# Kernel optimization log

Hardware: AMD Instinct MI355X
Metric: run time of the kernel (lower is better)

The kernel has to match this reference:

```python
import jax, jax.numpy as jnp
import numpy as np

T, B, I, H = 512, 256, 256, 256


def setup_inputs() -> dict:
    key = jax.random.key(0)
    ks = jax.random.split(key, 4)
    s = 1.0 / np.sqrt(I + H)  # fan-in scaling like nn.Linear default
    return {
        "x": jax.random.normal(ks[0], (T, B, I), dtype=jnp.float32),
        "h": jnp.zeros((B, H), dtype=jnp.float32),
        "Wz_w": jax.random.normal(ks[1], (H, I + H), dtype=jnp.float32) * s,
        "Wz_b": jnp.zeros((H,), dtype=jnp.float32),
        "Wr_w": jax.random.normal(ks[2], (H, I + H), dtype=jnp.float32) * s,
        "Wr_b": jnp.zeros((H,), dtype=jnp.float32),
        "W_w": jax.random.normal(ks[3], (H, I + H), dtype=jnp.float32) * s,
        "W_b": jnp.zeros((H,), dtype=jnp.float32),
    }


def reference(x, h, Wz_w, Wz_b, Wr_w, Wr_b, W_w, W_b):
    # x: [T, B, I], h: [B, H]. Gate input order is cat(h, x) as in the torch code.
    def step(h, xt):
        gate = jnp.concatenate([h, xt], axis=1)              # [B, H+I]
        zt = jax.nn.sigmoid(gate @ Wz_w.T + Wz_b)            # [B, H]
        rt = jax.nn.sigmoid(gate @ Wr_w.T + Wr_b)            # [B, H]
        cand_in = jnp.concatenate([rt * h, xt], axis=1)      # [B, H+I]
        ht = (1.0 - zt) * h + zt * jnp.tanh(cand_in @ W_w.T + W_b)
        return ht, ht

    h_final, hAll = jax.lax.scan(step, h, x)                 # hAll: [T, B, H]
    return hAll, h_final
```

## Files before the change

### kernel.cpp

```cpp
#include <hip/hip_runtime.h>


typedef float f32x4 __attribute__((ext_vector_type(4)));
typedef short bf16x8 __attribute__((ext_vector_type(8)));

__device__ __forceinline__ unsigned short f2bf(float f) {
  union { float f; unsigned int u; } v; v.f = f;
  unsigned int u = v.u + 0x7fffu + ((v.u >> 16) & 1u);
  return (unsigned short)(u >> 16);
}
__device__ __forceinline__ float u2f(unsigned int u) {
  union { unsigned int u; float f; } v; v.u = u; return v.f;
}
__device__ __forceinline__ unsigned int cvt_pk_bf16(float lo, float hi) {
  unsigned int r;
  asm("v_cvt_pk_bf16_f32 %0, %1, %2" : "=v"(r) : "v"(lo), "v"(hi));
  return r;
}
__device__ __forceinline__ float sigmoid_f(float x) {
  return __builtin_amdgcn_rcpf(1.f + __expf(-x));
}
__device__ __forceinline__ float tanh_f(float x) {
  float e = __expf(2.f * x);
  return 1.f - 2.f * __builtin_amdgcn_rcpf(e + 1.f);
}
__device__ __forceinline__ f32x4 unpk(uint2 gv) {
  f32x4 a;
  a[0] = u2f(gv.x << 16); a[1] = u2f(gv.x & 0xffff0000u);
  a[2] = u2f(gv.y << 16); a[3] = u2f(gv.y & 0xffff0000u);
  return a;
}

__global__ __launch_bounds__(256) void gru_gx_kernel(
    const float* __restrict__ x,
    const float* __restrict__ Wz, const float* __restrict__ Wr, const float* __restrict__ Wc,
    const float* __restrict__ bz, const float* __restrict__ br, const float* __restrict__ bc,
    unsigned short* __restrict__ gx)
{
  __shared__ __align__(16) unsigned short As[64][72];
  __shared__ __align__(16) unsigned short Bs[64][72];

  const int tid  = threadIdx.x;
  const int lane = tid & 63;
  const int wid  = tid >> 6;
  const int l15  = lane & 15;
  const int lg   = lane >> 4;
  const int m0   = blockIdx.x * 64;
  const int by   = blockIdx.y;
  const int gate = by >> 2;
  const int jb   = (by & 3) * 64;
  const float* W    = (gate == 0) ? Wz : ((gate == 1) ? Wr : Wc);
  const float* bias = (gate == 0) ? bz : ((gate == 1) ? br : bc);

  f32x4 acc[4];
  #pragma unroll
  for (int n = 0; n < 4; ++n) acc[n] = (f32x4){0.f, 0.f, 0.f, 0.f};

  for (int k0 = 0; k0 < 256; k0 += 64) {
    #pragma unroll
    for (int i = 0; i < 4; ++i) {
      int idx = tid + i * 256;
      int row = idx >> 4;
      int kq  = (idx & 15) << 2;
      float4 va = *(const float4*)(x + (size_t)(m0 + row) * 256 + k0 + kq);
      ushort4 ua; ua.x = f2bf(va.x); ua.y = f2bf(va.y); ua.z = f2bf(va.z); ua.w = f2bf(va.w);
      *(ushort4*)&As[row][kq] = ua;
      float4 vb = *(const float4*)(W + (size_t)(jb + row) * 512 + 256 + k0 + kq);
      ushort4 ub; ub.x = f2bf(vb.x); ub.y = f2bf(vb.y); ub.z = f2bf(vb.z); ub.w = f2bf(vb.w);
      *(ushort4*)&Bs[row][kq] = ub;
    }
    __syncthreads();
    #pragma unroll
    for (int ks = 0; ks < 64; ks += 32) {
      bf16x8 af = *(const bf16x8*)&As[wid * 16 + l15][ks + lg * 8];
      #pragma unroll
      for (int n = 0; n < 4; ++n) {
        bf16x8 bf = *(const bf16x8*)&Bs[n * 16 + l15][ks + lg * 8];
        acc[n] = __builtin_amdgcn_mfma_f32_16x16x32_bf16(af, bf, acc[n], 0, 0, 0);
      }
    }
    __syncthreads();
  }

  #pragma unroll
  for (int n = 0; n < 4; ++n) {
    float bv = bias[jb + n * 16 + l15];
    #pragma unroll
    for (int r = 0; r < 4; ++r) {
      As[wid * 16 + lg * 4 + r][n * 16 + l15] = f2bf(acc[n][r] + bv);
    }
  }
  __syncthreads();

  const int tt    = m0 >> 8;
  const int b0    = m0 & 255;
  const int jbase = by * 64;
  #pragma unroll
  for (int i = 0; i < 2; ++i) {
    int u    = tid + i * 256;
    int bg_l = u >> 7;
    int rem  = u & 127;
    int cb_l = rem >> 3;
    int bp   = rem & 7;
    int row0 = bg_l * 16 + bp * 2;
    uint2 lo = *(const uint2*)&As[row0][cb_l * 4];
    uint2 hi = *(const uint2*)&As[row0 + 1][cb_l * 4];
    uint4 val; val.x = lo.x; val.y = lo.y; val.z = hi.x; val.w = hi.y;
    size_t off = (((size_t)tt * 16 + (b0 >> 4) + bg_l) * 192 + (jbase >> 2) + cb_l) * 64
                 + (size_t)bp * 8;
    *(uint4*)(gx + off) = val;
  }
}

__global__ __launch_bounds__(512, 1) void gru_rec_kernel(
    const unsigned short* __restrict__ gx,
    const float* __restrict__ h0,
    const float* __restrict__ Wz, const float* __restrict__ Wr, const float* __restrict__ Wc,
    float* __restrict__ out)
{
  __shared__ __align__(16) float h_s[16][260];
  __shared__ __align__(16) float zt_s[16][260];
  __shared__ __align__(16) unsigned short hA[16][264];
  __shared__ __align__(16) unsigned short rhA[16][264];

  const int tid   = threadIdx.x;
  const int lane  = tid & 63;
  const int wid   = tid >> 6;
  const int l15   = lane & 15;
  const int lg    = lane >> 4;
  const int wg    = blockIdx.x;
  const int brow0 = wg * 16;

  bf16x8 w1[4][8];
  {
    const float* W  = (wid < 4) ? Wz : Wr;
    const int    cb = (wid & 3) * 64;
    #pragma unroll
    for (int n = 0; n < 4; ++n) {
      const int j = cb + n * 16 + l15;
      #pragma unroll
      for (int kk = 0; kk < 8; ++kk) {
        const int k = kk * 32 + lg * 8;
        const float* p = W + (size_t)j * 512 + k;
        float4 a = *(const float4*)p;
        float4 b = *(const float4*)(p + 4);
        bf16x8 f;
        f[0] = (short)f2bf(a.x); f[1] = (short)f2bf(a.y);
        f[2] = (short)f2bf(a.z); f[3] = (short)f2bf(a.w);
        f[4] = (short)f2bf(b.x); f[5] = (short)f2bf(b.y);
        f[6] = (short)f2bf(b.z); f[7] = (short)f2bf(b.w);
        w1[n][kk] = f;
      }
    }
  }
  bf16x8 w2[2][8];
  {
    const int cb = wid * 32;
    #pragma unroll
    for (int n = 0; n < 2; ++n) {
      const int j = cb + n * 16 + l15;
      #pragma unroll
      for (int kk = 0; kk < 8; ++kk) {
        const int k = kk * 32 + lg * 8;
        const float* p = Wc + (size_t)j * 512 + k;
        float4 a = *(const float4*)p;
        float4 b = *(const float4*)(p + 4);
        bf16x8 f;
        f[0] = (short)f2bf(a.x); f[1] = (short)f2bf(a.y);
        f[2] = (short)f2bf(a.z); f[3] = (short)f2bf(a.w);
        f[4] = (short)f2bf(b.x); f[5] = (short)f2bf(b.y);
        f[6] = (short)f2bf(b.z); f[7] = (short)f2bf(b.w);
        w2[n][kk] = f;
      }
    }
  }

  for (int idx = tid; idx < 16 * 256; idx += 512) {
    int r = idx >> 8, c = idx & 255;
    float v = h0[(size_t)(brow0 + r) * 256 + c];
    h_s[r][c] = v;
    hA[r][c]  = f2bf(v);
  }

  uint2 g1[4], g2[2];
  {
    const size_t tb = (size_t)wg * 12288;
    #pragma unroll
    for (int n = 0; n < 4; ++n)
      g1[n] = *(const uint2*)(gx + tb + (size_t)(wid * 16 + n * 4 + lg) * 64 + l15 * 4);
    #pragma unroll
    for (int n = 0; n < 2; ++n)
      g2[n] = *(const uint2*)(gx + tb + (size_t)(128 + wid * 8 + n * 4 + lg) * 64 + l15 * 4);
  }
  __syncthreads();

  for (int t = 0; t < 512; ++t) {
    const int tn = (t < 511) ? (t + 1) : 511;
    const size_t tbn = ((size_t)tn * 16 + wg) * 12288;

    const int cb1 = wid * 64;
    f32x4 acc[4];
    #pragma unroll
    for (int n = 0; n < 4; ++n) acc[n] = unpk(g1[n]);
    #pragma unroll
    for (int n = 0; n < 4; ++n)
      g1[n] = *(const uint2*)(gx + tbn + (size_t)(wid * 16 + n * 4 + lg) * 64 + l15 * 4);

    #pragma unroll
    for (int kk = 0; kk < 8; ++kk) {
      bf16x8 hf = *(const bf16x8*)&hA[l15][kk * 32 + lg * 8];
      #pragma unroll
      for (int n = 0; n < 4; ++n)
        acc[n] = __builtin_amdgcn_mfma_f32_16x16x32_bf16(w1[n][kk], hf, acc[n], 0, 0, 0);
    }
    if (wid < 4) {
      #pragma unroll
      for (int n = 0; n < 4; ++n) {
        const int c0 = cb1 + n * 16 + lg * 4;
        f32x4 zv;
        #pragma unroll
        for (int r = 0; r < 4; ++r) zv[r] = sigmoid_f(acc[n][r]);
        *(f32x4*)&zt_s[l15][c0] = zv;
      }
    } else {
      #pragma unroll
      for (int n = 0; n < 4; ++n) {
        const int c0h = (cb1 - 256) + n * 16 + lg * 4;
        f32x4 hv = *(const f32x4*)&h_s[l15][c0h];
        float rh0 = sigmoid_f(acc[n][0]) * hv[0];
        float rh1 = sigmoid_f(acc[n][1]) * hv[1];
        float rh2 = sigmoid_f(acc[n][2]) * hv[2];
        float rh3 = sigmoid_f(acc[n][3]) * hv[3];
        uint2 pk; pk.x = cvt_pk_bf16(rh0, rh1); pk.y = cvt_pk_bf16(rh2, rh3);
        *(uint2*)&rhA[l15][c0h] = pk;
      }
    }
    asm volatile("s_waitcnt lgkmcnt(0)" ::: "memory");
    __builtin_amdgcn_s_barrier();
    __builtin_amdgcn_sched_barrier(0);

    f32x4 acc2[2];
    #pragma unroll
    for (int n = 0; n < 2; ++n) acc2[n] = unpk(g2[n]);
    #pragma unroll
    for (int n = 0; n < 2; ++n)
      g2[n] = *(const uint2*)(gx + tbn + (size_t)(128 + wid * 8 + n * 4 + lg) * 64 + l15 * 4);

    #pragma unroll
    for (int kk = 0; kk < 8; ++kk) {
      bf16x8 rf = *(const bf16x8*)&rhA[l15][kk * 32 + lg * 8];
      #pragma unroll
      for (int n = 0; n < 2; ++n)
        acc2[n] = __builtin_amdgcn_mfma_f32_16x16x32_bf16(w2[n][kk], rf, acc2[n], 0, 0, 0);
    }
    #pragma unroll
    for (int n = 0; n < 2; ++n) {
      const int j0 = wid * 32 + n * 16 + lg * 4;
      f32x4 zv = *(const f32x4*)&zt_s[l15][j0];
      f32x4 hp = *(const f32x4*)&h_s[l15][j0];
      f32x4 ht;
      #pragma unroll
      for (int r = 0; r < 4; ++r) {
        float th = tanh_f(acc2[n][r]);
        ht[r] = hp[r] + zv[r] * (th - hp[r]);
      }
      *(f32x4*)(out + (size_t)t * 65536 + (size_t)(brow0 + l15) * 256 + j0) = ht;
      if (t == 511)
        *(f32x4*)(out + (size_t)33554432 + (size_t)(brow0 + l15) * 256 + j0) = ht;
      *(f32x4*)&h_s[l15][j0] = ht;
      uint2 pk; pk.x = cvt_pk_bf16(ht[0], ht[1]); pk.y = cvt_pk_bf16(ht[2], ht[3]);
      *(uint2*)&hA[l15][j0] = pk;
    }
    asm volatile("s_waitcnt lgkmcnt(0)" ::: "memory");
    __builtin_amdgcn_s_barrier();
    __builtin_amdgcn_sched_barrier(0);
  }
}

extern "C" void kernel_launch(void* const* d_in, const int* in_sizes, int n_in,
                              void* d_out, int out_size, void* d_ws, size_t ws_size,
                              hipStream_t stream) {
  const float* x  = (const float*)d_in[0];
  const float* h0 = (const float*)d_in[1];
  const float* Wz = (const float*)d_in[2];
  const float* bz = (const float*)d_in[3];
  const float* Wr = (const float*)d_in[4];
  const float* br = (const float*)d_in[5];
  const float* Wc = (const float*)d_in[6];
  const float* bc = (const float*)d_in[7];
  float* out = (float*)d_out;
  unsigned short* gxbuf = (unsigned short*)d_ws;

  dim3 gridA(2048, 12);
  gru_gx_kernel<<<gridA, 256, 0, stream>>>(x, Wz, Wr, Wc, bz, br, bc, gxbuf);
  gru_rec_kernel<<<16, 512, 0, stream>>>(gxbuf, h0, Wz, Wr, Wc, out);
}
```

Measured before the change: 1.272 ms.

## Store h in MFMA fragment order, split accumulator chains, raise MFMA priority

The bf16 hidden-state buffers hA and rhA now use an MFMA-fragment-ordered layout, so each lane reads its 8-element B operand as a contiguous 16-byte chunk at lane*8 instead of a strided row access. The K loop of both recurrent GEMMs is split into two independent accumulator chains that are summed before the activation, which shortens the dependent MFMA chain on the serial critical path. s_setprio raises wave priority around the MFMA blocks. The writes become scattered 8-byte stores through frag_off, and the extra accumulators raise register pressure.

```diff
diff --git a/kernel.cpp b/kernel.cpp
--- a/kernel.cpp
+++ b/kernel.cpp
@@ -29,6 +29,9 @@
   a[0] = u2f(gv.x << 16); a[1] = u2f(gv.x & 0xffff0000u);
   a[2] = u2f(gv.y << 16); a[3] = u2f(gv.y & 0xffff0000u);
   return a;
+}
+__device__ __forceinline__ int frag_off(int j, int b) {
+  return ((j >> 5) * 64 + ((j >> 3) & 3) * 16 + b) * 8 + (j & 7);
 }
 
 __global__ __launch_bounds__(256) void gru_gx_kernel(
@@ -120,8 +123,8 @@
 {
   __shared__ __align__(16) float h_s[16][260];
   __shared__ __align__(16) float zt_s[16][260];
-  __shared__ __align__(16) unsigned short hA[16][264];
-  __shared__ __align__(16) unsigned short rhA[16][264];
+  __shared__ __align__(16) unsigned short hA[4096];
+  __shared__ __align__(16) unsigned short rhA[4096];
 
   const int tid   = threadIdx.x;
   const int lane  = tid & 63;
@@ -179,7 +182,7 @@
     int r = idx >> 8, c = idx & 255;
     float v = h0[(size_t)(brow0 + r) * 256 + c];
     h_s[r][c] = v;
-    hA[r][c]  = f2bf(v);
+    hA[frag_off(c, r)] = f2bf(v);
   }
 
   uint2 g1[4], g2[2];
@@ -199,69 +202,98 @@
     const size_t tbn = ((size_t)tn * 16 + wg) * 12288;
 
     const int cb1 = wid * 64;
-    f32x4 acc[4];
-    #pragma unroll
-    for (int n = 0; n < 4; ++n) acc[n] = unpk(g1[n]);
+    f32x4 accA[4], accB[4];
+    #pragma unroll
+    for (int n = 0; n < 4; ++n) {
+      accA[n] = unpk(g1[n]);
+      accB[n] = (f32x4){0.f, 0.f, 0.f, 0.f};
+    }
     #pragma unroll
     for (int n = 0; n < 4; ++n)
       g1[n] = *(const uint2*)(gx + tbn + (size_t)(wid * 16 + n * 4 + lg) * 64 + l15 * 4);
 
-    #pragma unroll
-    for (int kk = 0; kk < 8; ++kk) {
-      bf16x8 hf = *(const bf16x8*)&hA[l15][kk * 32 + lg * 8];
+    __builtin_amdgcn_s_setprio(1);
+    #pragma unroll
+    for (int kk = 0; kk < 4; ++kk) {
+      bf16x8 hf = *(const bf16x8*)&hA[kk * 512 + lane * 8];
       #pragma unroll
       for (int n = 0; n < 4; ++n)
-        acc[n] = __builtin_amdgcn_mfma_f32_16x16x32_bf16(w1[n][kk], hf, acc[n], 0, 0, 0);
-    }
+        accA[n] = __builtin_amdgcn_mfma_f32_16x16x32_bf16(w1[n][kk], hf, accA[n], 0, 0, 0);
+    }
+    #pragma unroll
+    for (int kk = 4; kk < 8; ++kk) {
+      bf16x8 hf = *(const bf16x8*)&hA[kk * 512 + lane * 8];
+      #pragma unroll
+      for (int n = 0; n < 4; ++n)
+        accB[n] = __builtin_amdgcn_mfma_f32_16x16x32_bf16(w1[n][kk], hf, accB[n], 0, 0, 0);
+    }
+    __builtin_amdgcn_s_setprio(0);
+
     if (wid < 4) {
       #pragma unroll
       for (int n = 0; n < 4; ++n) {
         const int c0 = cb1 + n * 16 + lg * 4;
+        f32x4 s = accA[n] + accB[n];
         f32x4 zv;
         #pragma unroll
-        for (int r = 0; r < 4; ++r) zv[r] = sigmoid_f(acc[n][r]);
+        for (int r = 0; r < 4; ++r) zv[r] = sigmoid_f(s[r]);
         *(f32x4*)&zt_s[l15][c0] = zv;
       }
     } else {
       #pragma unroll
       for (int n = 0; n < 4; ++n) {
         const int c0h = (cb1 - 256) + n * 16 + lg * 4;
+        f32x4 s = accA[n] + accB[n];
         f32x4 hv = *(const f32x4*)&h_s[l15][c0h];
-        float rh0 = sigmoid_f(acc[n][0]) * hv[0];
-        float rh1 = sigmoid_f(acc[n][1]) * hv[1];
-        float rh2 = sigmoid_f(acc[n][2]) * hv[2];
-        float rh3 = sigmoid_f(acc[n][3]) * hv[3];
+        float rh0 = sigmoid_f(s[0]) * hv[0];
+        float rh1 = sigmoid_f(s[1]) * hv[1];
+        float rh2 = sigmoid_f(s[2]) * hv[2];
+        float rh3 = sigmoid_f(s[3]) * hv[3];
         uint2 pk; pk.x = cvt_pk_bf16(rh0, rh1); pk.y = cvt_pk_bf16(rh2, rh3);
-        *(uint2*)&rhA[l15][c0h] = pk;
+        *(uint2*)&rhA[frag_off(c0h, l15)] = pk;
       }
     }
     asm volatile("s_waitcnt lgkmcnt(0)" ::: "memory");
     __builtin_amdgcn_s_barrier();
     __builtin_amdgcn_sched_barrier(0);
 
-    f32x4 acc2[2];
-    #pragma unroll
-    for (int n = 0; n < 2; ++n) acc2[n] = unpk(g2[n]);
+    f32x4 acc2A[2], acc2B[2];
+    #pragma unroll
+    for (int n = 0; n < 2; ++n) {
+      acc2A[n] = unpk(g2[n]);
+      acc2B[n] = (f32x4){0.f, 0.f, 0.f, 0.f};
+    }
     #pragma unroll
     for (int n = 0; n < 2; ++n)
       g2[n] = *(const uint2*)(gx + tbn + (size_t)(128 + wid * 8 + n * 4 + lg) * 64 + l15 * 4);
 
-    #pragma unroll
-    for (int kk = 0; kk < 8; ++kk) {
-      bf16x8 rf = *(const bf16x8*)&rhA[l15][kk * 32 + lg * 8];
+    __builtin_amdgcn_s_setprio(1);
+    #pragma unroll
+    for (int kk = 0; kk < 4; ++kk) {
+      bf16x8 rf = *(const bf16x8*)&rhA[kk * 512 + lane * 8];
       #pragma unroll
       for (int n = 0; n < 2; ++n)
-        acc2[n] = __builtin_amdgcn_mfma_f32_16x16x32_bf16(w2[n][kk], rf, acc2[n], 0, 0, 0);
-    }
+        acc2A[n] = __builtin_amdgcn_mfma_f32_16x16x32_bf16(w2[n][kk], rf, acc2A[n], 0, 0, 0);
+    }
+    #pragma unroll
+    for (int kk = 4; kk < 8; ++kk) {
+      bf16x8 rf = *(const bf16x8*)&rhA[kk * 512 + lane * 8];
+      #pragma unroll
+      for (int n = 0; n < 2; ++n)
+        acc2B[n] = __builtin_amdgcn_mfma_f32_16x16x32_bf16(w2[n][kk], rf, acc2B[n], 0, 0, 0);
+    }
+    __builtin_amdgcn_s_setprio(0);
+
     #pragma unroll
     for (int n = 0; n < 2; ++n) {
       const int j0 = wid * 32 + n * 16 + lg * 4;
+      f32x4 s = acc2A[n] + acc2B[n];
       f32x4 zv = *(const f32x4*)&zt_s[l15][j0];
       f32x4 hp = *(const f32x4*)&h_s[l15][j0];
       f32x4 ht;
       #pragma unroll
       for (int r = 0; r < 4; ++r) {
-        float th = tanh_f(acc2[n][r]);
+        float th = tanh_f(s[r]);
         ht[r] = hp[r] + zv[r] * (th - hp[r]);
       }
       *(f32x4*)(out + (size_t)t * 65536 + (size_t)(brow0 + l15) * 256 + j0) = ht;
@@ -269,7 +301,7 @@
         *(f32x4*)(out + (size_t)33554432 + (size_t)(brow0 + l15) * 256 + j0) = ht;
       *(f32x4*)&h_s[l15][j0] = ht;
       uint2 pk; pk.x = cvt_pk_bf16(ht[0], ht[1]); pk.y = cvt_pk_bf16(ht[2], ht[3]);
-      *(uint2*)&hA[l15][j0] = pk;
+      *(uint2*)&hA[frag_off(j0, l15)] = pk;
     }
     asm volatile("s_waitcnt lgkmcnt(0)" ::: "memory");
     __builtin_amdgcn_s_barrier();
```

After: 1.971 ms. 1.55x slower.
